# Kernel optimization log

Measured on AMD Instinct MI355X. Metric: run time of the kernel, lower is better.

Reference implementation:

```python
import jax, jax.numpy as jnp
import numpy as np

IN_F, OUT_F, N_TOK = 4096, 4096, 8192

def setup_inputs() -> dict:
    key = jax.random.key(0)
    k1, k2, k3, k4, k5 = jax.random.split(key, 5)
    bound = 1.0 / np.sqrt(IN_F)  # kaiming_uniform-ish scale for mean, uniform for bias
    x = jax.random.normal(k1, (N_TOK, IN_F), dtype=jnp.float32)
    mean = jax.random.uniform(k2, (OUT_F, IN_F), minval=-bound, maxval=bound, dtype=jnp.float32)
    sigma = jax.random.uniform(k3, (OUT_F, IN_F), minval=0.05, maxval=0.2, dtype=jnp.float32)
    bias = jax.random.uniform(k4, (OUT_F,), minval=-bound, maxval=bound, dtype=jnp.float32)
    # uniform[-1, 1] noise matrix (torch init.uniform_(w, a=-1, b=1))
    noise = jax.random.uniform(k5, (OUT_F, IN_F), minval=-1.0, maxval=1.0, dtype=jnp.float32)
    sigma_mult = 2  # discrete bucket multiplier in {1, 2, 4}
    return {"x": x, "mean": mean, "sigma": sigma, "bias": bias, "noise": noise, "sigma_mult": sigma_mult}

def reference(x, mean, sigma, bias, noise, sigma_mult):
    # w = mean * (1 + noise * |sigma| * sigma_mult), then F.linear(x, w, bias) = x @ w.T + bias
    w = mean * (1.0 + noise * jnp.abs(sigma) * sigma_mult)  # [out, in]
    return jnp.einsum('ti,oi->to', x, w) + bias
```

## Files before the change

kernel.cpp:

```cpp
#include <hip/hip_runtime.h>
#include <hip/hip_bf16.h>

#define M_TOK 8192
#define N_OUT 4096
#define K_IN  4096

typedef __attribute__((ext_vector_type(8))) short bf16x8;
typedef __attribute__((ext_vector_type(4))) float f32x4;
typedef unsigned short u16;

__device__ static inline u16 f2bf(float f) {
    union { float f; unsigned int u; } v; v.f = f;
    unsigned int u = v.u;
    u += 0x7FFFu + ((u >> 16) & 1u);
    return (u16)(u >> 16);
}

__device__ static inline void load_lds16(const void* g, void* l) {
    __builtin_amdgcn_global_load_lds(
        (const __attribute__((address_space(1))) unsigned int*)g,
        (__attribute__((address_space(3))) unsigned int*)l,
        16, 0, 0);
}

__global__ void prep_kernel(const float* __restrict__ x,
                            const float* __restrict__ mean,
                            const float* __restrict__ sigma,
                            const float* __restrict__ noise,
                            const int* __restrict__ smult,
                            u16* __restrict__ xb, u16* __restrict__ wb) {
    if (blockIdx.x < 2048) {
        const int n4 = (M_TOK * K_IN) / 4;
        int i = blockIdx.x * blockDim.x + threadIdx.x;
        const int stride = 2048 * 256;
        for (int e = i; e < n4; e += stride) {
            float4 v = reinterpret_cast<const float4*>(x)[e];
            ushort4 o;
            o.x = f2bf(v.x); o.y = f2bf(v.y); o.z = f2bf(v.z); o.w = f2bf(v.w);
            reinterpret_cast<ushort4*>(xb)[e] = o;
        }
    } else {
        const float sm = (float)(*smult);
        const int n4 = (N_OUT * K_IN) / 4;
        int i = (blockIdx.x - 2048) * blockDim.x + threadIdx.x;
        const int stride = 1024 * 256;
        for (int e = i; e < n4; e += stride) {
            float4 m = reinterpret_cast<const float4*>(mean)[e];
            float4 s = reinterpret_cast<const float4*>(sigma)[e];
            float4 z = reinterpret_cast<const float4*>(noise)[e];
            ushort4 o;
            o.x = f2bf(m.x * (1.0f + z.x * fabsf(s.x) * sm));
            o.y = f2bf(m.y * (1.0f + z.y * fabsf(s.y) * sm));
            o.z = f2bf(m.z * (1.0f + z.z * fabsf(s.z) * sm));
            o.w = f2bf(m.w * (1.0f + z.w * fabsf(s.w) * sm));
            reinterpret_cast<ushort4*>(wb)[e] = o;
        }
    }
}


#define BARM()   { __builtin_amdgcn_s_barrier(); asm volatile("" ::: "memory"); }
#define SCHED0() __builtin_amdgcn_sched_barrier(0)
#define VMC0()   asm volatile("s_waitcnt vmcnt(0)" ::: "memory")

#define DS_A4(AR, MG, AB) \
  _Pragma("unroll") for (int m_ = 0; m_ < 4; ++m_) { \
    AR[m_][0] = *reinterpret_cast<const bf16x8*>((AB) + ((MG)+m_)*1024 + aoff0); \
    AR[m_][1] = *reinterpret_cast<const bf16x8*>((AB) + ((MG)+m_)*1024 + aoff1); }

#define DS_B2(BR, NG, BB) \
  _Pragma("unroll") for (int n_ = 0; n_ < 2; ++n_) { \
    BR[n_][0] = *reinterpret_cast<const bf16x8*>((BB) + ((NG)+n_)*1024 + aoff0); \
    BR[n_][1] = *reinterpret_cast<const bf16x8*>((BB) + ((NG)+n_)*1024 + aoff1); }

#define QUAD(MG, NG, AR, BR) \
  __builtin_amdgcn_s_setprio(1); \
  _Pragma("unroll") for (int m_ = 0; m_ < 4; ++m_) \
  _Pragma("unroll") for (int n_ = 0; n_ < 2; ++n_) { \
    acc[(MG)+m_][(NG)+n_] = __builtin_amdgcn_mfma_f32_16x16x32_bf16( \
        AR[m_][0], BR[n_][0], acc[(MG)+m_][(NG)+n_], 0, 0, 0); \
    acc[(MG)+m_][(NG)+n_] = __builtin_amdgcn_mfma_f32_16x16x32_bf16( \
        AR[m_][1], BR[n_][1], acc[(MG)+m_][(NG)+n_], 0, 0, 0); } \
  __builtin_amdgcn_s_setprio(0);

#define STAGE_A(T, H, BUF) { \
  const u16* g_ = Abase + (size_t)((H)*128 + srow) * K_IN + (T)*64 + sxcol; \
  load_lds16(g_, smem + (BUF)*32768 + (H)*8192 + tid*8); \
  load_lds16(g_ + (size_t)64*K_IN, smem + (BUF)*32768 + (H)*8192 + 4096 + tid*8); }

#define STAGE_B(T, H, BUF) { \
  const u16* g_ = Bbase + (size_t)((H)*128 + srow) * K_IN + (T)*64 + sxcol; \
  load_lds16(g_, smem + (BUF)*32768 + 16384 + (H)*8192 + tid*8); \
  load_lds16(g_ + (size_t)64*K_IN, smem + (BUF)*32768 + 16384 + (H)*8192 + 4096 + tid*8); }

#define TILE(T, RB, WB) { \
  const int tn_ = ((T) < 63) ? (T) + 1 : 63; \
  STAGE_A(tn_, 0, WB); STAGE_A(tn_, 1, WB); \
  STAGE_B(tn_, 0, WB); STAGE_B(tn_, 1, WB); \
  SCHED0(); \
  const u16* A_ = smem + (RB)*32768 + wm*8192; \
  const u16* B_ = smem + (RB)*32768 + 16384 + (wn>>1)*8192 + (wn&1)*4096; \
  DS_A4(aR, 0, A_); DS_B2(bA, 0, B_); DS_B2(bB, 2, B_); \
  QUAD(0, 0, aR, bA); QUAD(0, 2, aR, bB); \
  DS_A4(aR, 4, A_); \
  QUAD(4, 2, aR, bB); QUAD(4, 0, aR, bA); \
  VMC0(); BARM(); }

__global__ __launch_bounds__(512, 2)
void gemm_bias_kernel(const u16* __restrict__ A, const u16* __restrict__ B,
                      const float* __restrict__ bias, float* __restrict__ C) {
    __shared__ u16 smem[65536];

    const int tid   = threadIdx.x;
    const int lane  = tid & 63;
    const int wid   = tid >> 6;
    const int wm    = wid >> 2;
    const int wn    = wid & 3;
    const int la_lo = lane & 15;
    const int la_hi = lane >> 4;

    const int bid = blockIdx.x;
    const int xcd = bid & 7;
    const int c   = bid >> 3;
    const int r   = c >> 5;
    const int s   = c & 31;
    const int bm  = xcd * 4 + (s & 3);
    const int bn  = r * 8 + (s >> 2);
    const int brow = bm * 256;
    const int bcol = bn * 256;

    const u16* Abase = A + (size_t)brow * K_IN;
    const u16* Bbase = B + (size_t)bcol * K_IN;

    const int srow  = tid >> 3;
    const int sxcol = ((tid & 7) ^ (srow & 7)) * 8;

    const int xorr  = la_lo & 7;
    const int aoff0 = la_lo * 64 + ((la_hi    ) ^ xorr) * 8;
    const int aoff1 = la_lo * 64 + ((la_hi + 4) ^ xorr) * 8;

    f32x4 acc[8][4];
    #pragma unroll
    for (int m = 0; m < 8; ++m)
        #pragma unroll
        for (int n = 0; n < 4; ++n)
            acc[m][n] = (f32x4){0.f, 0.f, 0.f, 0.f};

    bf16x8 aR[4][2], bA[2][2], bB[2][2];

    STAGE_A(0, 0, 0); STAGE_A(0, 1, 0);
    STAGE_B(0, 0, 0); STAGE_B(0, 1, 0);
    VMC0(); BARM();

    for (int i = 0; i < 32; ++i) {
        TILE(2 * i,     0, 1);
        TILE(2 * i + 1, 1, 0);
    }

    const int crow0 = brow + wm * 128;
    const int ccol0 = bcol + wn * 64;
    #pragma unroll
    for (int n = 0; n < 4; ++n) {
        const int col = ccol0 + n * 16 + la_lo;
        const float bv = bias[col];
        #pragma unroll
        for (int m = 0; m < 8; ++m) {
            #pragma unroll
            for (int rr = 0; rr < 4; ++rr) {
                const int row = crow0 + m * 16 + la_hi * 4 + rr;
                C[(size_t)row * N_OUT + col] = acc[m][n][rr] + bv;
            }
        }
    }
}

extern "C" void kernel_launch(void* const* d_in, const int* in_sizes, int n_in,
                              void* d_out, int out_size, void* d_ws, size_t ws_size,
                              hipStream_t stream) {
    const float* x     = (const float*)d_in[0];
    const float* mean  = (const float*)d_in[1];
    const float* sigma = (const float*)d_in[2];
    const float* bias  = (const float*)d_in[3];
    const float* noise = (const float*)d_in[4];
    const int*   smult = (const int*)d_in[5];
    float* out = (float*)d_out;

    const size_t x_elems = (size_t)M_TOK * K_IN;
    const size_t w_elems = (size_t)N_OUT * K_IN;
    const size_t need = (x_elems + w_elems) * sizeof(u16);
    if (ws_size < need) return;

    u16* xb = (u16*)d_ws;
    u16* wb = xb + x_elems;

    prep_kernel<<<3072, 256, 0, stream>>>(x, mean, sigma, noise, smult, xb, wb);
    gemm_bias_kernel<<<512, 512, 0, stream>>>(xb, wb, bias, out);
}
```

Before: 318.9 us.

## Shrink GEMM block tile to 128x128 with 4 waves and 64x64 warp tiles

Replaces the 256x256 block tile (8 waves, 128x64 per wave) with a 128x128 tile using 4 waves of 64x64 each, launching 2048 blocks of 256 threads. The LDS footprint halves and the staging and fragment-load macros are rewritten for the smaller tile. The aim is more blocks in flight and better load balance across CUs. In exchange, arithmetic intensity per block drops, so global and LDS traffic per FLOP rises.

```diff
diff --git a/kernel.cpp b/kernel.cpp
--- a/kernel.cpp
+++ b/kernel.cpp
@@ -63,71 +63,65 @@
 #define SCHED0() __builtin_amdgcn_sched_barrier(0)
 #define VMC0()   asm volatile("s_waitcnt vmcnt(0)" ::: "memory")
 
-#define DS_A4(AR, MG, AB) \
-  _Pragma("unroll") for (int m_ = 0; m_ < 4; ++m_) { \
-    AR[m_][0] = *reinterpret_cast<const bf16x8*>((AB) + ((MG)+m_)*1024 + aoff0); \
-    AR[m_][1] = *reinterpret_cast<const bf16x8*>((AB) + ((MG)+m_)*1024 + aoff1); }
+#define LDA(KK) \
+  _Pragma("unroll") for (int m_ = 0; m_ < 4; ++m_) \
+    aR[m_] = *reinterpret_cast<const bf16x8*>(A_ + m_*1024 + aoff[KK]);
 
-#define DS_B2(BR, NG, BB) \
-  _Pragma("unroll") for (int n_ = 0; n_ < 2; ++n_) { \
-    BR[n_][0] = *reinterpret_cast<const bf16x8*>((BB) + ((NG)+n_)*1024 + aoff0); \
-    BR[n_][1] = *reinterpret_cast<const bf16x8*>((BB) + ((NG)+n_)*1024 + aoff1); }
+#define LDB(KK) \
+  _Pragma("unroll") for (int n_ = 0; n_ < 4; ++n_) \
+    bR[n_] = *reinterpret_cast<const bf16x8*>(B_ + n_*1024 + aoff[KK]);
 
-#define QUAD(MG, NG, AR, BR) \
+#define MF16() \
   __builtin_amdgcn_s_setprio(1); \
   _Pragma("unroll") for (int m_ = 0; m_ < 4; ++m_) \
-  _Pragma("unroll") for (int n_ = 0; n_ < 2; ++n_) { \
-    acc[(MG)+m_][(NG)+n_] = __builtin_amdgcn_mfma_f32_16x16x32_bf16( \
-        AR[m_][0], BR[n_][0], acc[(MG)+m_][(NG)+n_], 0, 0, 0); \
-    acc[(MG)+m_][(NG)+n_] = __builtin_amdgcn_mfma_f32_16x16x32_bf16( \
-        AR[m_][1], BR[n_][1], acc[(MG)+m_][(NG)+n_], 0, 0, 0); } \
+  _Pragma("unroll") for (int n_ = 0; n_ < 4; ++n_) \
+    acc[m_][n_] = __builtin_amdgcn_mfma_f32_16x16x32_bf16( \
+        aR[m_], bR[n_], acc[m_][n_], 0, 0, 0); \
   __builtin_amdgcn_s_setprio(0);
 
-#define STAGE_A(T, H, BUF) { \
-  const u16* g_ = Abase + (size_t)((H)*128 + srow) * K_IN + (T)*64 + sxcol; \
-  load_lds16(g_, smem + (BUF)*32768 + (H)*8192 + tid*8); \
-  load_lds16(g_ + (size_t)64*K_IN, smem + (BUF)*32768 + (H)*8192 + 4096 + tid*8); }
+#define STAGE_OP(T, Q, BUF, GBASE, LOFF) { \
+  const u16* g_ = (GBASE) + (size_t)((Q)*32 + srow) * K_IN + (T)*64 + sxcol; \
+  load_lds16(g_, smem + (BUF)*16384 + (LOFF) + (Q)*2048 + tid*8); }
 
-#define STAGE_B(T, H, BUF) { \
-  const u16* g_ = Bbase + (size_t)((H)*128 + srow) * K_IN + (T)*64 + sxcol; \
-  load_lds16(g_, smem + (BUF)*32768 + 16384 + (H)*8192 + tid*8); \
-  load_lds16(g_ + (size_t)64*K_IN, smem + (BUF)*32768 + 16384 + (H)*8192 + 4096 + tid*8); }
+#define STAGE_ALL(T, BUF) \
+  STAGE_OP(T, 0, BUF, Abase, 0)    STAGE_OP(T, 1, BUF, Abase, 0) \
+  STAGE_OP(T, 2, BUF, Abase, 0)    STAGE_OP(T, 3, BUF, Abase, 0) \
+  STAGE_OP(T, 0, BUF, Bbase, 8192) STAGE_OP(T, 1, BUF, Bbase, 8192) \
+  STAGE_OP(T, 2, BUF, Bbase, 8192) STAGE_OP(T, 3, BUF, Bbase, 8192)
 
 #define TILE(T, RB, WB) { \
   const int tn_ = ((T) < 63) ? (T) + 1 : 63; \
-  STAGE_A(tn_, 0, WB); STAGE_A(tn_, 1, WB); \
-  STAGE_B(tn_, 0, WB); STAGE_B(tn_, 1, WB); \
+  STAGE_ALL(tn_, WB); \
   SCHED0(); \
-  const u16* A_ = smem + (RB)*32768 + wm*8192; \
-  const u16* B_ = smem + (RB)*32768 + 16384 + (wn>>1)*8192 + (wn&1)*4096; \
-  DS_A4(aR, 0, A_); DS_B2(bA, 0, B_); DS_B2(bB, 2, B_); \
-  QUAD(0, 0, aR, bA); QUAD(0, 2, aR, bB); \
-  DS_A4(aR, 4, A_); \
-  QUAD(4, 2, aR, bB); QUAD(4, 0, aR, bA); \
+  const u16* A_ = smem + (RB)*16384 +        wr*4096; \
+  const u16* B_ = smem + (RB)*16384 + 8192 + wc*4096; \
+  { bf16x8 aR[4], bR[4]; \
+    LDA(0); LDB(0); MF16(); \
+    LDA(1); LDB(1); MF16(); } \
   VMC0(); BARM(); }
 
-__global__ __launch_bounds__(512, 2)
+__global__ __launch_bounds__(256, 2)
 void gemm_bias_kernel(const u16* __restrict__ A, const u16* __restrict__ B,
                       const float* __restrict__ bias, float* __restrict__ C) {
-    __shared__ u16 smem[65536];
+    __shared__ u16 smem[32768];
 
     const int tid   = threadIdx.x;
     const int lane  = tid & 63;
     const int wid   = tid >> 6;
-    const int wm    = wid >> 2;
-    const int wn    = wid & 3;
+    const int wr    = wid >> 1;
+    const int wc    = wid & 1;
     const int la_lo = lane & 15;
     const int la_hi = lane >> 4;
 
     const int bid = blockIdx.x;
     const int xcd = bid & 7;
     const int c   = bid >> 3;
-    const int r   = c >> 5;
-    const int s   = c & 31;
-    const int bm  = xcd * 4 + (s & 3);
-    const int bn  = r * 8 + (s >> 2);
-    const int brow = bm * 256;
-    const int bcol = bn * 256;
+    const int r   = c >> 6;
+    const int s   = c & 63;
+    const int bm  = xcd * 8 + (s & 7);
+    const int bn  = r * 8 + (s >> 3);
+    const int brow = bm * 128;
+    const int bcol = bn * 128;
 
     const u16* Abase = A + (size_t)brow * K_IN;
     const u16* Bbase = B + (size_t)bcol * K_IN;
@@ -135,21 +129,19 @@
     const int srow  = tid >> 3;
     const int sxcol = ((tid & 7) ^ (srow & 7)) * 8;
 
-    const int xorr  = la_lo & 7;
-    const int aoff0 = la_lo * 64 + ((la_hi    ) ^ xorr) * 8;
-    const int aoff1 = la_lo * 64 + ((la_hi + 4) ^ xorr) * 8;
+    const int xorr = la_lo & 7;
+    int aoff[2];
+    aoff[0] = la_lo * 64 + ((la_hi    ) ^ xorr) * 8;
+    aoff[1] = la_lo * 64 + ((la_hi + 4) ^ xorr) * 8;
 
-    f32x4 acc[8][4];
+    f32x4 acc[4][4];
     #pragma unroll
-    for (int m = 0; m < 8; ++m)
+    for (int m = 0; m < 4; ++m)
         #pragma unroll
         for (int n = 0; n < 4; ++n)
             acc[m][n] = (f32x4){0.f, 0.f, 0.f, 0.f};
 
-    bf16x8 aR[4][2], bA[2][2], bB[2][2];
-
-    STAGE_A(0, 0, 0); STAGE_A(0, 1, 0);
-    STAGE_B(0, 0, 0); STAGE_B(0, 1, 0);
+    STAGE_ALL(0, 0);
     VMC0(); BARM();
 
     for (int i = 0; i < 32; ++i) {
@@ -157,14 +149,14 @@
         TILE(2 * i + 1, 1, 0);
     }
 
-    const int crow0 = brow + wm * 128;
-    const int ccol0 = bcol + wn * 64;
+    const int crow0 = brow + wr * 64;
+    const int ccol0 = bcol + wc * 64;
     #pragma unroll
     for (int n = 0; n < 4; ++n) {
         const int col = ccol0 + n * 16 + la_lo;
         const float bv = bias[col];
         #pragma unroll
-        for (int m = 0; m < 8; ++m) {
+        for (int m = 0; m < 4; ++m) {
             #pragma unroll
             for (int rr = 0; rr < 4; ++rr) {
                 const int row = crow0 + m * 16 + la_hi * 4 + rr;
@@ -194,5 +186,5 @@
     u16* wb = xb + x_elems;
 
     prep_kernel<<<3072, 256, 0, stream>>>(x, mean, sigma, noise, smult, xb, wb);
-    gemm_bias_kernel<<<512, 512, 0, stream>>>(xb, wb, bias, out);
+    gemm_bias_kernel<<<2048, 256, 0, stream>>>(xb, wb, bias, out);
 }
```

Measured after the change: 341.8 us. 1.07x slower.

## Pre-pack weights into MFMA fragment layout and load B directly to registers

Applied to the files above, without the earlier changes.

The prep kernel now writes the perturbed bf16 weight matrix in a packed layout that matches MFMA B-fragment order, so each lane of the GEMM can fetch its B operand with direct global vector loads instead of staging it through LDS. LDS is then used only for A, in a four-buffer ring with deeper prefetch (two tiles ahead), and the wait is relaxed to vmcnt(8) instead of a full drain. The aim is to cut LDS traffic and barrier stalls and to overlap more memory with MFMA. The cost is more registers for the double-buffered B fragments and B reuse now relying on L2 rather than shared memory across waves, which could hurt occupancy or cache behaviour.

```diff
diff --git a/kernel.cpp b/kernel.cpp
--- a/kernel.cpp
+++ b/kernel.cpp
@@ -41,19 +41,31 @@
         }
     } else {
         const float sm = (float)(*smult);
-        const int n4 = (N_OUT * K_IN) / 4;
-        int i = (blockIdx.x - 2048) * blockDim.x + threadIdx.x;
+        const int NB8 = N_OUT * (K_IN / 8);
+        int g = (blockIdx.x - 2048) * blockDim.x + threadIdx.x;
         const int stride = 1024 * 256;
-        for (int e = i; e < n4; e += stride) {
-            float4 m = reinterpret_cast<const float4*>(mean)[e];
-            float4 s = reinterpret_cast<const float4*>(sigma)[e];
-            float4 z = reinterpret_cast<const float4*>(noise)[e];
-            ushort4 o;
-            o.x = f2bf(m.x * (1.0f + z.x * fabsf(s.x) * sm));
-            o.y = f2bf(m.y * (1.0f + z.y * fabsf(s.y) * sm));
-            o.z = f2bf(m.z * (1.0f + z.z * fabsf(s.z) * sm));
-            o.w = f2bf(m.w * (1.0f + z.w * fabsf(s.w) * sm));
-            reinterpret_cast<ushort4*>(wb)[e] = o;
+        for (; g < NB8; g += stride) {
+            const int o  = g >> 9;
+            const int i8 = g & 511;
+            const size_t src = (size_t)o * K_IN + (size_t)i8 * 8;
+            float4 m0 = *reinterpret_cast<const float4*>(mean  + src);
+            float4 m1 = *reinterpret_cast<const float4*>(mean  + src + 4);
+            float4 s0 = *reinterpret_cast<const float4*>(sigma + src);
+            float4 s1 = *reinterpret_cast<const float4*>(sigma + src + 4);
+            float4 z0 = *reinterpret_cast<const float4*>(noise + src);
+            float4 z1 = *reinterpret_cast<const float4*>(noise + src + 4);
+            bf16x8 w;
+            w[0] = (short)f2bf(m0.x * (1.0f + z0.x * fabsf(s0.x) * sm));
+            w[1] = (short)f2bf(m0.y * (1.0f + z0.y * fabsf(s0.y) * sm));
+            w[2] = (short)f2bf(m0.z * (1.0f + z0.z * fabsf(s0.z) * sm));
+            w[3] = (short)f2bf(m0.w * (1.0f + z0.w * fabsf(s0.w) * sm));
+            w[4] = (short)f2bf(m1.x * (1.0f + z1.x * fabsf(s1.x) * sm));
+            w[5] = (short)f2bf(m1.y * (1.0f + z1.y * fabsf(s1.y) * sm));
+            w[6] = (short)f2bf(m1.z * (1.0f + z1.z * fabsf(s1.z) * sm));
+            w[7] = (short)f2bf(m1.w * (1.0f + z1.w * fabsf(s1.w) * sm));
+            const size_t dst = (size_t)(o >> 4) * 65536 + (size_t)(i8 >> 2) * 512
+                             + (size_t)((o & 15) | ((i8 & 3) << 4)) * 8;
+            *reinterpret_cast<bf16x8*>(wb + dst) = w;
         }
     }
 }
@@ -61,53 +73,57 @@
 
 #define BARM()   { __builtin_amdgcn_s_barrier(); asm volatile("" ::: "memory"); }
 #define SCHED0() __builtin_amdgcn_sched_barrier(0)
-#define VMC0()   asm volatile("s_waitcnt vmcnt(0)" ::: "memory")
-
-#define DS_A4(AR, MG, AB) \
+#define VMC8()   asm volatile("s_waitcnt vmcnt(8)" ::: "memory")
+
+#define DS_A4(AR, AB) \
   _Pragma("unroll") for (int m_ = 0; m_ < 4; ++m_) { \
-    AR[m_][0] = *reinterpret_cast<const bf16x8*>((AB) + ((MG)+m_)*1024 + aoff0); \
-    AR[m_][1] = *reinterpret_cast<const bf16x8*>((AB) + ((MG)+m_)*1024 + aoff1); }
-
-#define DS_B2(BR, NG, BB) \
-  _Pragma("unroll") for (int n_ = 0; n_ < 2; ++n_) { \
-    BR[n_][0] = *reinterpret_cast<const bf16x8*>((BB) + ((NG)+n_)*1024 + aoff0); \
-    BR[n_][1] = *reinterpret_cast<const bf16x8*>((BB) + ((NG)+n_)*1024 + aoff1); }
-
-#define QUAD(MG, NG, AR, BR) \
+    AR[m_][0] = *reinterpret_cast<const bf16x8*>((AB) + m_*1024 + aoff0); \
+    AR[m_][1] = *reinterpret_cast<const bf16x8*>((AB) + m_*1024 + aoff1); }
+
+#define OCT8(MG, BS) \
   __builtin_amdgcn_s_setprio(1); \
   _Pragma("unroll") for (int m_ = 0; m_ < 4; ++m_) \
-  _Pragma("unroll") for (int n_ = 0; n_ < 2; ++n_) { \
-    acc[(MG)+m_][(NG)+n_] = __builtin_amdgcn_mfma_f32_16x16x32_bf16( \
-        AR[m_][0], BR[n_][0], acc[(MG)+m_][(NG)+n_], 0, 0, 0); \
-    acc[(MG)+m_][(NG)+n_] = __builtin_amdgcn_mfma_f32_16x16x32_bf16( \
-        AR[m_][1], BR[n_][1], acc[(MG)+m_][(NG)+n_], 0, 0, 0); } \
+  _Pragma("unroll") for (int n_ = 0; n_ < 4; ++n_) { \
+    acc[(MG)+m_][n_] = __builtin_amdgcn_mfma_f32_16x16x32_bf16( \
+        aR[m_][0], BS[n_][0], acc[(MG)+m_][n_], 0, 0, 0); \
+    acc[(MG)+m_][n_] = __builtin_amdgcn_mfma_f32_16x16x32_bf16( \
+        aR[m_][1], BS[n_][1], acc[(MG)+m_][n_], 0, 0, 0); } \
   __builtin_amdgcn_s_setprio(0);
 
-#define STAGE_A(T, H, BUF) { \
-  const u16* g_ = Abase + (size_t)((H)*128 + srow) * K_IN + (T)*64 + sxcol; \
-  load_lds16(g_, smem + (BUF)*32768 + (H)*8192 + tid*8); \
-  load_lds16(g_ + (size_t)64*K_IN, smem + (BUF)*32768 + (H)*8192 + 4096 + tid*8); }
-
-#define STAGE_B(T, H, BUF) { \
-  const u16* g_ = Bbase + (size_t)((H)*128 + srow) * K_IN + (T)*64 + sxcol; \
-  load_lds16(g_, smem + (BUF)*32768 + 16384 + (H)*8192 + tid*8); \
-  load_lds16(g_ + (size_t)64*K_IN, smem + (BUF)*32768 + 16384 + (H)*8192 + 4096 + tid*8); }
-
-#define TILE(T, RB, WB) { \
-  const int tn_ = ((T) < 63) ? (T) + 1 : 63; \
-  STAGE_A(tn_, 0, WB); STAGE_A(tn_, 1, WB); \
-  STAGE_B(tn_, 0, WB); STAGE_B(tn_, 1, WB); \
+#define STAGE_A(T, BUF) { \
+  const u16* g_ = Abase + (size_t)srow * K_IN + (T)*64 + sxcol; \
+  load_lds16(g_,                     smem + (BUF)*16384 +         tid*8); \
+  load_lds16(g_ + (size_t) 64*K_IN,  smem + (BUF)*16384 +  4096 + tid*8); \
+  load_lds16(g_ + (size_t)128*K_IN,  smem + (BUF)*16384 +  8192 + tid*8); \
+  load_lds16(g_ + (size_t)192*K_IN,  smem + (BUF)*16384 + 12288 + tid*8); }
+
+#define LDBG(DST, T) \
+  _Pragma("unroll") for (int n_ = 0; n_ < 4; ++n_) \
+  _Pragma("unroll") for (int k_ = 0; k_ < 2; ++k_) \
+    DST[n_][k_] = *reinterpret_cast<const bf16x8*>( \
+        Bpk + (size_t)n_ * 65536 + (size_t)(T) * 1024 + k_ * 512);
+
+#define CTILE(RB, BS) { \
+  const u16* A_ = smem + (RB)*16384 + wm*8192; \
+  DS_A4(aR, A_); \
+  OCT8(0, BS); \
+  DS_A4(aR, A_ + 4096); \
+  OCT8(4, BS); }
+
+#define WINDOW(T0, RB0, RB1, WB0, WB1) { \
+  const int t2_ = ((T0)+2 < 64) ? (T0)+2 : 63; \
+  const int t3_ = ((T0)+3 < 64) ? (T0)+3 : 63; \
+  const int tb1_ = ((T0)+1 < 64) ? (T0)+1 : 63; \
+  STAGE_A(t2_, WB0); STAGE_A(t3_, WB1); \
+  LDBG(bB, tb1_); \
+  CTILE(RB0, bA); \
   SCHED0(); \
-  const u16* A_ = smem + (RB)*32768 + wm*8192; \
-  const u16* B_ = smem + (RB)*32768 + 16384 + (wn>>1)*8192 + (wn&1)*4096; \
-  DS_A4(aR, 0, A_); DS_B2(bA, 0, B_); DS_B2(bB, 2, B_); \
-  QUAD(0, 0, aR, bA); QUAD(0, 2, aR, bB); \
-  DS_A4(aR, 4, A_); \
-  QUAD(4, 2, aR, bB); QUAD(4, 0, aR, bA); \
-  VMC0(); BARM(); }
+  LDBG(bA, t2_); \
+  CTILE(RB1, bB); \
+  VMC8(); BARM(); }
 
 __global__ __launch_bounds__(512, 2)
-void gemm_bias_kernel(const u16* __restrict__ A, const u16* __restrict__ B,
+void gemm_bias_kernel(const u16* __restrict__ A, const u16* __restrict__ Bp,
                       const float* __restrict__ bias, float* __restrict__ C) {
     __shared__ u16 smem[65536];
 
@@ -130,7 +146,7 @@
     const int bcol = bn * 256;
 
     const u16* Abase = A + (size_t)brow * K_IN;
-    const u16* Bbase = B + (size_t)bcol * K_IN;
+    const u16* Bpk = Bp + (size_t)(bn * 16 + wn * 4) * 65536 + (size_t)lane * 8;
 
     const int srow  = tid >> 3;
     const int sxcol = ((tid & 7) ^ (srow & 7)) * 8;
@@ -146,15 +162,16 @@
         for (int n = 0; n < 4; ++n)
             acc[m][n] = (f32x4){0.f, 0.f, 0.f, 0.f};
 
-    bf16x8 aR[4][2], bA[2][2], bB[2][2];
-
-    STAGE_A(0, 0, 0); STAGE_A(0, 1, 0);
-    STAGE_B(0, 0, 0); STAGE_B(0, 1, 0);
-    VMC0(); BARM();
-
-    for (int i = 0; i < 32; ++i) {
-        TILE(2 * i,     0, 1);
-        TILE(2 * i + 1, 1, 0);
+    bf16x8 aR[4][2];
+    bf16x8 bA[4][2], bB[4][2];
+
+    STAGE_A(0, 0); STAGE_A(1, 1);
+    LDBG(bA, 0);
+    VMC8(); BARM();
+
+    for (int i = 0; i < 16; ++i) {
+        WINDOW(4 * i,     0, 1, 2, 3);
+        WINDOW(4 * i + 2, 2, 3, 0, 1);
     }
 
     const int crow0 = brow + wm * 128;
```

Measured after the change: 356.3 us. +11.7%, slower.
